# Optimization experiments

Hardware: AMD Instinct MI355X
Metric: run time of the kernel (lower is better)

The kernel has to match this reference:

```python
import jax, jax.numpy as jnp
import numpy as np

DIM = 1024
NUM_HEADS = 16
HEAD_DIM = DIM // NUM_HEADS
MLP_HIDDEN = 4 * DIM
TAU = 2.0
EPS = 1e-6
ALPHA_INIT = 0.01


def _xavier(key, out_f, in_f):
    limit = float(np.sqrt(6.0 / (in_f + out_f)))
    return jax.random.uniform(key, (out_f, in_f), jnp.float32, -limit, limit)


def setup_inputs() -> dict:
    key = jax.random.key(0)
    ks = jax.random.split(key, 10)
    B, Lq, Lkv = 4, 512, 2048
    return {
        "q_tokens": jax.random.normal(ks[0], (B, Lq, DIM), jnp.float32),
        "kv_tokens": jax.random.normal(ks[1], (B, Lkv, DIM), jnp.float32),
        "q_ln_w": jnp.ones((DIM,), jnp.float32),
        "q_ln_b": jnp.zeros((DIM,), jnp.float32),
        "kv_ln_w": jnp.ones((DIM,), jnp.float32),
        "kv_ln_b": jnp.zeros((DIM,), jnp.float32),
        "mlp_ln_w": jnp.ones((DIM,), jnp.float32),
        "mlp_ln_b": jnp.zeros((DIM,), jnp.float32),
        "Wq": _xavier(ks[2], DIM, DIM),
        "Wk": _xavier(ks[3], DIM, DIM),
        "Wv": _xavier(ks[4], DIM, DIM),
        "Wo": _xavier(ks[5], DIM, DIM),
        "bo": jnp.zeros((DIM,), jnp.float32),
        "fc1_w": _xavier(ks[6], MLP_HIDDEN, DIM),
        "fc1_b": jnp.zeros((MLP_HIDDEN,), jnp.float32),
        "fc2_w": _xavier(ks[7], DIM, MLP_HIDDEN),
        "fc2_b": jnp.zeros((DIM,), jnp.float32),
        "alpha_attn": jnp.full((1,), ALPHA_INIT, jnp.float32),
        "alpha_mlp": jnp.full((1,), ALPHA_INIT, jnp.float32),
    }


def _ln(x, w, b):
    mu = jnp.mean(x, axis=-1, keepdims=True)
    var = jnp.var(x, axis=-1, keepdims=True)
    return (x - mu) * jax.lax.rsqrt(var + EPS) * w + b


def _l2norm(x):
    # matches torch F.normalize: x / max(||x||, eps)
    n = jnp.sqrt(jnp.sum(x * x, axis=-1, keepdims=True))
    return x / jnp.maximum(n, EPS)


def reference(q_tokens, kv_tokens, q_ln_w, q_ln_b, kv_ln_w, kv_ln_b,
              mlp_ln_w, mlp_ln_b, Wq, Wk, Wv, Wo, bo,
              fc1_w, fc1_b, fc2_w, fc2_b, alpha_attn, alpha_mlp):
    B, Lq, D = q_tokens.shape
    q = _ln(q_tokens, q_ln_w, q_ln_b) @ Wq.T  # [B,Lq,D]
    kvn = _ln(kv_tokens, kv_ln_w, kv_ln_b)
    k = kvn @ Wk.T
    v = kvn @ Wv.T
    # split heads -> [B,H,L,hd]
    q = q.reshape(B, Lq, NUM_HEADS, HEAD_DIM)
    k = k.reshape(B, -1, NUM_HEADS, HEAD_DIM)
    v = v.reshape(B, -1, NUM_HEADS, HEAD_DIM)
    q = _l2norm(q)
    k = _l2norm(k)
    scores = jnp.einsum('bqhd,bkhd->bhqk', q, k) / TAU
    attn = jax.nn.softmax(scores, axis=-1)
    ctx = jnp.einsum('bhqk,bkhd->bqhd', attn, v).reshape(B, Lq, D)
    ctx = ctx @ Wo.T + bo
    out = q_tokens + alpha_attn * ctx
    h = _ln(out, mlp_ln_w, mlp_ln_b)
    h = jax.nn.gelu(h @ fc1_w.T + fc1_b, approximate=False)
    h = h @ fc2_w.T + fc2_b
    return out + alpha_mlp * h
```

## Files before the change

### kernel.cpp

```cpp
#include <hip/hip_runtime.h>


typedef __attribute__((ext_vector_type(8))) short short8_t;
typedef __attribute__((ext_vector_type(4))) float f32x4_t;

#define WSCALE 16.0f
#define OSC (1.0f / 16.0f)

__device__ __forceinline__ float b2f(short s) {
    union { float f; unsigned u; } c;
    c.u = ((unsigned)(unsigned short)s) << 16;
    return c.f;
}
__device__ __forceinline__ short f2b(float f) {
    union { float f; unsigned u; } c;
    c.f = f;
    unsigned u = c.u;
    unsigned r = (u + 0x7FFFu + ((u >> 16) & 1u)) >> 16;
    return (short)r;
}
__device__ __forceinline__ unsigned f2f8_pk4(float a, float b, float c, float d) {
    int lo = __builtin_amdgcn_cvt_pk_fp8_f32(a, b, 0, false);
    return (unsigned)__builtin_amdgcn_cvt_pk_fp8_f32(c, d, lo, true);
}
__device__ __forceinline__ unsigned char f2f8(float a) {
    return (unsigned char)(__builtin_amdgcn_cvt_pk_fp8_f32(a, a, 0, false) & 0xff);
}

__device__ __forceinline__ void gload16(const void* g, void* l) {
    __builtin_amdgcn_global_load_lds(
        (const __attribute__((address_space(1))) void*)g,
        (__attribute__((address_space(3))) void*)l, 16, 0, 0);
}

template <int OUT8>
__device__ __forceinline__ void ln_row(
    const float* __restrict__ x, const float* __restrict__ w,
    const float* __restrict__ bia, void* __restrict__ y,
    int row, int tid, float* red)
{
    const float4 t = *(const float4*)(x + (size_t)row * 1024 + tid * 4);
    float v[4] = {t.x, t.y, t.z, t.w};
    float s = v[0] + v[1] + v[2] + v[3];
    float s2 = v[0]*v[0] + v[1]*v[1] + v[2]*v[2] + v[3]*v[3];
    #pragma unroll
    for (int off = 1; off < 64; off <<= 1) {
        s  += __shfl_xor(s, off);
        s2 += __shfl_xor(s2, off);
    }
    const int wave = tid >> 6, lane = tid & 63;
    if (lane == 0) { red[wave] = s; red[4 + wave] = s2; }
    __syncthreads();
    s  = red[0] + red[1] + red[2] + red[3];
    s2 = red[4] + red[5] + red[6] + red[7];
    const float mu  = s * (1.0f / 1024.0f);
    const float var = s2 * (1.0f / 1024.0f) - mu * mu;
    const float rstd = rsqrtf(var + 1e-6f);
    const float4 wv = *(const float4*)(w + tid * 4);
    const float4 bv = *(const float4*)(bia + tid * 4);
    const float o0 = (v[0] - mu) * rstd * wv.x + bv.x;
    const float o1 = (v[1] - mu) * rstd * wv.y + bv.y;
    const float o2 = (v[2] - mu) * rstd * wv.z + bv.z;
    const float o3 = (v[3] - mu) * rstd * wv.w + bv.w;
    if (OUT8) {
        ((unsigned*)y)[(size_t)row * 256 + tid] = f2f8_pk4(o0, o1, o2, o3);
    } else {
        short4 o;
        o.x = f2b(o0); o.y = f2b(o1); o.z = f2b(o2); o.w = f2b(o3);
        *(short4*)((short*)y + (size_t)row * 1024 + tid * 4) = o;
    }
}

__global__ __launch_bounds__(256) void prep_kernel(
    const float* __restrict__ qt, const float* __restrict__ kvt,
    const float* __restrict__ qlw, const float* __restrict__ qlb,
    const float* __restrict__ klw, const float* __restrict__ klb,
    short* __restrict__ qn, unsigned char* __restrict__ kvn8,
    const float* __restrict__ Wq, const float* __restrict__ Wo,
    const float* __restrict__ Wk, const float* __restrict__ Wv,
    const float* __restrict__ fc1w, const float* __restrict__ fc2w,
    short* __restrict__ Wq_b, short* __restrict__ Wo_b,
    unsigned char* __restrict__ Wkv8,
    unsigned char* __restrict__ fc1_8, unsigned char* __restrict__ fc2_8)
{
    __shared__ float red[8];
    const int bid = blockIdx.x, tid = threadIdx.x;
    if (bid < 2048) {
        ln_row<0>(qt, qlw, qlb, qn, bid, tid, red);
    } else if (bid < 10240) {
        ln_row<1>(kvt, klw, klb, kvn8, bid - 2048, tid, red);
    } else {
        int f = (bid - 10240) * 256 + tid;
        if (f < 524288) {
            const float* src = (f < 262144) ? Wq : Wo;
            short* dst = (f < 262144) ? Wq_b : Wo_b;
            const int off = f & 262143;
            const float4 v = ((const float4*)src)[off];
            short4 o;
            o.x = f2b(v.x); o.y = f2b(v.y); o.z = f2b(v.z); o.w = f2b(v.w);
            ((short4*)dst)[off] = o;
        } else {
            const float* src; unsigned* dst; int off;
            if (f < 1048576) {
                off = f - 524288;
                src = (off < 262144) ? Wk : Wv;
                dst = (unsigned*)Wkv8;
                if (off >= 262144) { src = Wv; }
                const int so = (off < 262144) ? off : off - 262144;
                const float4 v = ((const float4*)src)[so];
                dst[off] = f2f8_pk4(v.x * WSCALE, v.y * WSCALE,
                                    v.z * WSCALE, v.w * WSCALE);
                return;
            } else if (f < 2097152) {
                off = f - 1048576; src = fc1w; dst = (unsigned*)fc1_8;
            } else {
                off = f - 2097152; src = fc2w; dst = (unsigned*)fc2_8;
            }
            const float4 v = ((const float4*)src)[off];
            dst[off] = f2f8_pk4(v.x * WSCALE, v.y * WSCALE,
                                v.z * WSCALE, v.w * WSCALE);
        }
    }
}

__global__ __launch_bounds__(256) void ln8_kernel(
    const float* __restrict__ x, const float* __restrict__ w,
    const float* __restrict__ bia, unsigned char* __restrict__ y)
{
    __shared__ float red[8];
    ln_row<1>(x, w, bia, y, blockIdx.x, threadIdx.x, red);
}

template <int EPI, int BM>
__global__ __launch_bounds__(256) void gemm_bt_kernel(
    const short* __restrict__ A, const short* __restrict__ W,
    int M, int N, int Ks, int Kst,
    const float* __restrict__ bias,
    const float* __restrict__ resF,
    const float* __restrict__ alpha,
    short* __restrict__ out16,
    float* __restrict__ outF)
{
    constexpr int MI = BM / 32;
    __shared__ __attribute__((aligned(16))) short As[2][BM * 64];
    __shared__ __attribute__((aligned(16))) short Bs[2][128 * 64];
    const int bm = blockIdx.y * BM, bn = blockIdx.x * 128;
    const int tid = threadIdx.x;
    const int wave = tid >> 6, lane = tid & 63;
    const int wm = (wave >> 1) * (BM / 2), wn = (wave & 1) * 64;
    const int l15 = lane & 15, quad = lane >> 4;
    const int l7 = l15 & 7;

    f32x4_t acc[MI][4];
    #pragma unroll
    for (int mi = 0; mi < MI; ++mi)
        #pragma unroll
        for (int ni = 0; ni < 4; ++ni)
            acc[mi][ni] = (f32x4_t){0.f, 0.f, 0.f, 0.f};

    auto stage = [&](int buf, int k0) {
        #pragma unroll
        for (int c = 0; c < BM / 32; ++c) {
            const int o = c * 4096 + tid * 16;
            const int row = o >> 7;
            const int g = ((o >> 4) & 7) ^ (row & 7);
            gload16(A + (size_t)(bm + row) * Kst + k0 + g * 8,
                    (char*)As[buf] + c * 4096 + wave * 1024);
        }
        #pragma unroll
        for (int c = 0; c < 4; ++c) {
            const int o = c * 4096 + tid * 16;
            const int row = o >> 7;
            const int g = ((o >> 4) & 7) ^ (row & 7);
            gload16(W + (size_t)(bn + row) * Kst + k0 + g * 8,
                    (char*)Bs[buf] + c * 4096 + wave * 1024);
        }
    };

    const int nIter = Ks >> 6;
    stage(0, 0);
    for (int it = 0; it < nIter; ++it) {
        const int buf = it & 1;
        __syncthreads();
        if (it + 1 < nIter) stage(buf ^ 1, (it + 1) * 64);
        #pragma unroll
        for (int h = 0; h < 2; ++h) {
            const int fg = (((h << 2) | quad) ^ l7) * 8;
            short8_t af[MI], bf[4];
            #pragma unroll
            for (int mi = 0; mi < MI; ++mi)
                af[mi] = *(const short8_t*)&As[buf][(wm + mi * 16 + l15) * 64 + fg];
            #pragma unroll
            for (int ni = 0; ni < 4; ++ni)
                bf[ni] = *(const short8_t*)&Bs[buf][(wn + ni * 16 + l15) * 64 + fg];
            #pragma unroll
            for (int mi = 0; mi < MI; ++mi)
                #pragma unroll
                for (int ni = 0; ni < 4; ++ni)
                    acc[mi][ni] = __builtin_amdgcn_mfma_f32_16x16x32_bf16(
                        af[mi], bf[ni], acc[mi][ni], 0, 0, 0);
        }
    }

    if (EPI == 4) {
        #pragma unroll
        for (int mi = 0; mi < MI; ++mi)
            #pragma unroll
            for (int r = 0; r < 4; ++r) {
                float s = 0.f;
                #pragma unroll
                for (int ni = 0; ni < 4; ++ni) {
                    const float x = acc[mi][ni][r];
                    s += x * x;
                }
                s += __shfl_xor(s, 1); s += __shfl_xor(s, 2);
                s += __shfl_xor(s, 4); s += __shfl_xor(s, 8);
                const float sc = 1.0f / fmaxf(sqrtf(s), 1e-6f);
                #pragma unroll
                for (int ni = 0; ni < 4; ++ni) acc[mi][ni][r] *= sc;
            }
    }

    const float a = (EPI == 1) ? alpha[0] : 0.f;
    #pragma unroll
    for (int mi = 0; mi < MI; ++mi) {
        #pragma unroll
        for (int ni = 0; ni < 4; ++ni) {
            const int n = bn + wn + ni * 16 + l15;
            const float bb = (EPI == 1) ? bias[n] : 0.f;
            #pragma unroll
            for (int r = 0; r < 4; ++r) {
                const int m = bm + wm + mi * 16 + (quad << 2) + r;
                const float x = acc[mi][ni][r];
                if (EPI == 4) {
                    out16[(size_t)m * N + n] = f2b(x);
                } else {
                    const size_t idx = (size_t)m * N + n;
                    outF[idx] = resF[idx] + a * (x + bb);
                }
            }
        }
    }
}

template <int EPI, int BM>
__global__ __launch_bounds__(256) void gemm_f8_kernel(
    const unsigned char* __restrict__ A, const unsigned char* __restrict__ W,
    int M, int N, int Ks, int Kst,
    const float* __restrict__ bias,
    unsigned char* __restrict__ out8,
    short* __restrict__ out16,
    float* __restrict__ outF)
{
    constexpr int MI = BM / 32;
    __shared__ __attribute__((aligned(16))) unsigned char pool[2 * BM * 128 + 2 * 128 * 128];
    auto AsBuf = [&](int b) { return pool + b * (BM * 128); };
    auto BsBuf = [&](int b) { return pool + 2 * BM * 128 + b * (128 * 128); };
    const int bm = blockIdx.y * BM, bn = blockIdx.x * 128;
    const size_t kbase = (size_t)blockIdx.z * Ks;
    const int tid = threadIdx.x;
    const int wave = tid >> 6, lane = tid & 63;
    const int wm = (wave >> 1) * (BM / 2), wn = (wave & 1) * 64;
    const int l15 = lane & 15, quad = lane >> 4;
    const int l7 = l15 & 7;

    f32x4_t acc[MI][4];
    #pragma unroll
    for (int mi = 0; mi < MI; ++mi)
        #pragma unroll
        for (int ni = 0; ni < 4; ++ni)
            acc[mi][ni] = (f32x4_t){0.f, 0.f, 0.f, 0.f};

    auto stage = [&](int buf, int k0) {
        #pragma unroll
        for (int c = 0; c < BM / 32; ++c) {
            const int o = c * 4096 + tid * 16;
            const int row = o >> 7;
            const int g = ((o >> 4) & 7) ^ (row & 7);
            gload16(A + (size_t)(bm + row) * Kst + kbase + k0 + g * 16,
                    (char*)AsBuf(buf) + c * 4096 + wave * 1024);
        }
        #pragma unroll
        for (int c = 0; c < 4; ++c) {
            const int o = c * 4096 + tid * 16;
            const int row = o >> 7;
            const int g = ((o >> 4) & 7) ^ (row & 7);
            gload16(W + (size_t)(bn + row) * Kst + kbase + k0 + g * 16,
                    (char*)BsBuf(buf) + c * 4096 + wave * 1024);
        }
    };

    const int nIter = Ks >> 7;
    stage(0, 0);
    for (int it = 0; it < nIter; ++it) {
        const int buf = it & 1;
        __syncthreads();
        if (it + 1 < nIter) stage(buf ^ 1, (it + 1) * 128);
        #pragma unroll
        for (int ks = 0; ks < 4; ++ks) {
            const int fo = ((((ks << 1) | (quad >> 1)) ^ l7) << 4) + (quad & 1) * 8;
            long af[MI], bf[4];
            #pragma unroll
            for (int mi = 0; mi < MI; ++mi)
                af[mi] = *(const long*)(AsBuf(buf) + (wm + mi * 16 + l15) * 128 + fo);
            #pragma unroll
            for (int ni = 0; ni < 4; ++ni)
                bf[ni] = *(const long*)(BsBuf(buf) + (wn + ni * 16 + l15) * 128 + fo);
            #pragma unroll
            for (int mi = 0; mi < MI; ++mi)
                #pragma unroll
                for (int ni = 0; ni < 4; ++ni)
                    acc[mi][ni] = __builtin_amdgcn_mfma_f32_16x16x32_fp8_fp8(
                        af[mi], bf[ni], acc[mi][ni], 0, 0, 0);
        }
    }

    if (EPI == 8) {
        const bool isK = (bn < 1024);
        if (isK) {
            #pragma unroll
            for (int mi = 0; mi < MI; ++mi)
                #pragma unroll
                for (int r = 0; r < 4; ++r) {
                    float s = 0.f;
                    #pragma unroll
                    for (int ni = 0; ni < 4; ++ni) {
                        const float x = acc[mi][ni][r];
                        s += x * x;
                    }
                    s += __shfl_xor(s, 1); s += __shfl_xor(s, 2);
                    s += __shfl_xor(s, 4); s += __shfl_xor(s, 8);
                    const float sc = 1.0f / fmaxf(sqrtf(s), 1e-6f);
                    #pragma unroll
                    for (int ni = 0; ni < 4; ++ni) acc[mi][ni][r] *= sc;
                }
        }
        __syncthreads();
        short* Ct = (short*)pool;
        constexpr int LDC = 136;
        if (isK) {
            #pragma unroll
            for (int mi = 0; mi < MI; ++mi)
                #pragma unroll
                for (int ni = 0; ni < 4; ++ni) {
                    const int n = wn + ni * 16 + l15;
                    #pragma unroll
                    for (int r = 0; r < 4; ++r)
                        Ct[(wm + mi * 16 + (quad << 2) + r) * LDC + n] =
                            f2b(acc[mi][ni][r]);
                }
        } else {
            #pragma unroll
            for (int mi = 0; mi < MI; ++mi)
                #pragma unroll
                for (int ni = 0; ni < 4; ++ni) {
                    short4 pk;
                    pk.x = f2b(acc[mi][ni][0] * OSC);
                    pk.y = f2b(acc[mi][ni][1] * OSC);
                    pk.z = f2b(acc[mi][ni][2] * OSC);
                    pk.w = f2b(acc[mi][ni][3] * OSC);
                    *(short4*)&Ct[(wn + ni * 16 + l15) * LDC +
                                  wm + mi * 16 + (quad << 2)] = pk;
                }
        }
        __syncthreads();
        const int b_ = bm >> 11;
        const int kv0 = bm & 2047;
        #pragma unroll
        for (int p = 0; p < 8; ++p) {
            const int idx = p * 256 + tid;
            const int row = idx >> 4, ch = idx & 15;
            const short8_t v = *(const short8_t*)&Ct[row * LDC + ch * 8];
            if (isK) {
                const int hh = (bn >> 6) + (ch >> 3);
                *(short8_t*)&out16[(size_t)((b_ * 16 + hh) * 2048 + kv0 + row) * 64 +
                                   (ch & 7) * 8] = v;
            } else {
                const int nn = bn - 1024 + row;
                *(short8_t*)&((short*)outF)[(size_t)((b_ * 16 + (nn >> 6)) * 64 +
                                            (nn & 63)) * 2048 + kv0 + ch * 8] = v;
            }
        }
        return;
    }

    if (EPI == 2) {
        __syncthreads();
        unsigned char* C8 = (unsigned char*)pool;
        constexpr int LDC8 = 144;
        #pragma unroll
        for (int mi = 0; mi < MI; ++mi)
            #pragma unroll
            for (int ni = 0; ni < 4; ++ni) {
                const int n = wn + ni * 16 + l15;
                const float bb = bias[bn + n];
                #pragma unroll
                for (int r = 0; r < 4; ++r) {
                    const float t = acc[mi][ni][r] * OSC + bb;
                    C8[(wm + mi * 16 + (quad << 2) + r) * LDC8 + n] =
                        f2f8(0.5f * t * (1.0f + erff(t * 0.70710678118f)));
                }
            }
        __syncthreads();
        #pragma unroll
        for (int p = 0; p < 4; ++p) {
            const int idx = p * 256 + tid;
            const int row = idx >> 3, ch = idx & 7;
            const f32x4_t v = *(const f32x4_t*)&C8[row * LDC8 + ch * 16];
            *(f32x4_t*)&out8[(size_t)(bm + row) * N + bn + ch * 16] = v;
        }
        return;
    }

    #pragma unroll
    for (int mi = 0; mi < MI; ++mi) {
        #pragma unroll
        for (int ni = 0; ni < 4; ++ni) {
            const int n = bn + wn + ni * 16 + l15;
            #pragma unroll
            for (int r = 0; r < 4; ++r) {
                const int m = bm + wm + mi * 16 + (quad << 2) + r;
                outF[(size_t)blockIdx.z * M * N + (size_t)m * N + n] =
                    acc[mi][ni][r];
            }
        }
    }
}

__global__ __launch_bounds__(256) void reduce4_kernel(
    const float* __restrict__ parts, const float* __restrict__ resF,
    const float* __restrict__ bias, const float* __restrict__ alpha,
    float* __restrict__ out)
{
    const int i = blockIdx.x * 256 + threadIdx.x;
    const size_t MN4 = (size_t)2048 * 1024 / 4;
    const float a = alpha[0];
    const float4 b4 = ((const float4*)bias)[i & 255];
    float4 s = ((const float4*)parts)[i];
    const float4 p1 = ((const float4*)parts)[MN4 + i];
    const float4 p2 = ((const float4*)parts)[2 * MN4 + i];
    const float4 p3 = ((const float4*)parts)[3 * MN4 + i];
    const float4 rv = ((const float4*)resF)[i];
    float4 o;
    o.x = rv.x + a * ((s.x + p1.x + p2.x + p3.x) * OSC + b4.x);
    o.y = rv.y + a * ((s.y + p1.y + p2.y + p3.y) * OSC + b4.y);
    o.z = rv.z + a * ((s.z + p1.z + p2.z + p3.z) * OSC + b4.z);
    o.w = rv.w + a * ((s.w + p1.w + p2.w + p3.w) * OSC + b4.w);
    ((float4*)out)[i] = o;
}

__global__ __launch_bounds__(256) void attn_kernel(
    const short* __restrict__ q, const short* __restrict__ khd,
    const short* __restrict__ vhd, float* __restrict__ o0,
    float* __restrict__ o1, float* __restrict__ lpart)
{
    const int h  = blockIdx.x;
    const int b  = blockIdx.y;
    const int qt = blockIdx.z >> 1;
    const int sp = blockIdx.z & 1;
    const int tid = threadIdx.x;
    const int wave = tid >> 6, lane = tid & 63;
    const int l15 = lane & 15, quad = lane >> 4;
    const int q0 = qt * 64 + wave * 16;
    const int t0 = sp * 16;

    __shared__ __attribute__((aligned(16))) short Ks[2][4096];
    __shared__ __attribute__((aligned(16))) short Vs[2][4096];
    __shared__ __attribute__((aligned(16))) short P[4][1152];

    const short* qbase = q + (size_t)(b * 512 + q0 + l15) * 1024 + h * 64 + quad * 8;
    const short8_t aq0 = *(const short8_t*)(qbase);
    const short8_t aq1 = *(const short8_t*)(qbase + 32);

    const short* kbase = khd + (size_t)(b * 16 + h) * 2048 * 64;
    const short* vbase = vhd + (size_t)(b * 16 + h) * 64 * 2048;

    const int swz = l15 & 7;
    const int g0 = (quad ^ swz) * 8;
    const int g1 = ((quad ^ swz) ^ 4) * 8;

    auto stage = [&](int buf, int t) {
        #pragma unroll
        for (int c = 0; c < 2; ++c) {
            const int o = c * 4096 + tid * 16;
            const int row = o >> 7;
            const int g = ((o >> 4) & 7) ^ (row & 7);
            gload16(kbase + (size_t)(t * 64 + row) * 64 + g * 8,
                    (char*)Ks[buf] + c * 4096 + wave * 1024);
            gload16(vbase + (size_t)row * 2048 + t * 64 + g * 8,
                    (char*)Vs[buf] + c * 4096 + wave * 1024);
        }
    };

    const short8_t ones = {(short)0x3F80, (short)0x3F80, (short)0x3F80,
                           (short)0x3F80, (short)0x3F80, (short)0x3F80,
                           (short)0x3F80, (short)0x3F80};

    f32x4_t oacc[4];
    #pragma unroll
    for (int u = 0; u < 4; ++u) oacc[u] = (f32x4_t){0.f, 0.f, 0.f, 0.f};
    f32x4_t lacc = (f32x4_t){0.f, 0.f, 0.f, 0.f};

    stage(0, t0);
    for (int tt = 0; tt < 16; ++tt) {
        const int buf = tt & 1;
        __syncthreads();
        if (tt + 1 < 16) stage(buf ^ 1, t0 + tt + 1);

        f32x4_t s[4];
        #pragma unroll
        for (int ss = 0; ss < 4; ++ss) {
            const int R = ss * 16 + l15;
            const short8_t bk0 = *(const short8_t*)&Ks[buf][R * 64 + g0];
            const short8_t bk1 = *(const short8_t*)&Ks[buf][R * 64 + g1];
            f32x4_t a = (f32x4_t){0.f, 0.f, 0.f, 0.f};
            a = __builtin_amdgcn_mfma_f32_16x16x32_bf16(aq0, bk0, a, 0, 0, 0);
            a = __builtin_amdgcn_mfma_f32_16x16x32_bf16(aq1, bk1, a, 0, 0, 0);
            s[ss] = a;
        }
        #pragma unroll
        for (int ss = 0; ss < 4; ++ss)
            #pragma unroll
            for (int r = 0; r < 4; ++r) {
                const float p = __expf(s[ss][r] * 0.5f);
                P[wave][(quad * 4 + r) * 72 + ss * 16 + l15] = f2b(p);
            }
        const short8_t ap0 = *(const short8_t*)&P[wave][l15 * 72 + quad * 8];
        const short8_t ap1 = *(const short8_t*)&P[wave][l15 * 72 + 32 + quad * 8];
        lacc = __builtin_amdgcn_mfma_f32_16x16x32_bf16(ap0, ones, lacc, 0, 0, 0);
        lacc = __builtin_amdgcn_mfma_f32_16x16x32_bf16(ap1, ones, lacc, 0, 0, 0);
        #pragma unroll
        for (int u = 0; u < 4; ++u) {
            const int R = u * 16 + l15;
            const short8_t bv0 = *(const short8_t*)&Vs[buf][R * 64 + g0];
            const short8_t bv1 = *(const short8_t*)&Vs[buf][R * 64 + g1];
            oacc[u] = __builtin_amdgcn_mfma_f32_16x16x32_bf16(ap0, bv0, oacc[u], 0, 0, 0);
            oacc[u] = __builtin_amdgcn_mfma_f32_16x16x32_bf16(ap1, bv1, oacc[u], 0, 0, 0);
        }
    }

    float* ob = sp ? o1 : o0;
    float* lb = lpart + (size_t)sp * 2048 * 16;
    #pragma unroll
    for (int u = 0; u < 4; ++u)
        #pragma unroll
        for (int r = 0; r < 4; ++r)
            ob[(size_t)(b * 512 + q0 + quad * 4 + r) * 1024 + h * 64 + u * 16 + l15] =
                oacc[u][r];
    if (l15 == 0) {
        #pragma unroll
        for (int r = 0; r < 4; ++r)
            lb[(size_t)(b * 512 + q0 + quad * 4 + r) * 16 + h] = lacc[r];
    }
}

__global__ __launch_bounds__(256) void attn_combine_kernel(
    const float* __restrict__ o0, const float* __restrict__ o1,
    const float* __restrict__ lpart, short* __restrict__ ctx)
{
    const int i = blockIdx.x * 256 + threadIdx.x;
    const int row = i >> 8;
    const int h = (i & 255) >> 4;
    const float l = lpart[row * 16 + h] + lpart[2048 * 16 + row * 16 + h];
    const float inv = 1.0f / l;
    const float4 a = ((const float4*)o0)[i];
    const float4 c = ((const float4*)o1)[i];
    short4 o;
    o.x = f2b((a.x + c.x) * inv);
    o.y = f2b((a.y + c.y) * inv);
    o.z = f2b((a.z + c.z) * inv);
    o.w = f2b((a.w + c.w) * inv);
    ((short4*)ctx)[i] = o;
}

extern "C" void kernel_launch(void* const* d_in, const int* in_sizes, int n_in,
                              void* d_out, int out_size, void* d_ws, size_t ws_size,
                              hipStream_t stream)
{
    const float* q_tokens  = (const float*)d_in[0];
    const float* kv_tokens = (const float*)d_in[1];
    const float* q_ln_w    = (const float*)d_in[2];
    const float* q_ln_b    = (const float*)d_in[3];
    const float* kv_ln_w   = (const float*)d_in[4];
    const float* kv_ln_b   = (const float*)d_in[5];
    const float* mlp_ln_w  = (const float*)d_in[6];
    const float* mlp_ln_b  = (const float*)d_in[7];
    const float* Wq        = (const float*)d_in[8];
    const float* Wk        = (const float*)d_in[9];
    const float* Wv        = (const float*)d_in[10];
    const float* Wo        = (const float*)d_in[11];
    const float* bo        = (const float*)d_in[12];
    const float* fc1_w     = (const float*)d_in[13];
    const float* fc1_b     = (const float*)d_in[14];
    const float* fc2_w     = (const float*)d_in[15];
    const float* fc2_b     = (const float*)d_in[16];
    const float* alpha_attn = (const float*)d_in[17];
    const float* alpha_mlp  = (const float*)d_in[18];

    char* ws = (char*)d_ws;
    const size_t MB = (size_t)1 << 20;
    short* khd    = (short*)(ws);
    short* vhd    = (short*)(ws + 16 * MB);
    float* parts  = (float*)(ws);
    unsigned char* kvn8 = (unsigned char*)(ws + 32 * MB);
    float* attn_o0 = (float*)(ws + 32 * MB);
    unsigned char* h1   = (unsigned char*)(ws + 32 * MB);
    short* qn     = (short*)(ws + 40 * MB);
    short* qbuf   = (short*)(ws + 44 * MB);
    short* ctx    = (short*)(ws + 48 * MB);
    float* aout   = (float*)(ws + 52 * MB);
    float* attn_o1 = (float*)(ws + 52 * MB);
    unsigned char* hn8 = (unsigned char*)(ws + 60 * MB);
    float* attn_l  = (float*)(ws + 60 * MB);
    short* Wq_b   = (short*)(ws + 62 * MB);
    short* Wo_b   = (short*)(ws + 64 * MB);
    unsigned char* Wkv8  = (unsigned char*)(ws + 66 * MB);
    unsigned char* fc1_8 = (unsigned char*)(ws + 68 * MB);
    unsigned char* fc2_8 = (unsigned char*)(ws + 72 * MB);

    prep_kernel<<<22528, 256, 0, stream>>>(
        q_tokens, kv_tokens, q_ln_w, q_ln_b, kv_ln_w, kv_ln_b, qn, kvn8,
        Wq, Wo, Wk, Wv, fc1_w, fc2_w,
        Wq_b, Wo_b, Wkv8, fc1_8, fc2_8);

    gemm_bt_kernel<4, 64><<<dim3(8, 32), 256, 0, stream>>>(
        qn, Wq_b, 2048, 1024, 1024, 1024, nullptr, nullptr, nullptr, qbuf, nullptr);
    gemm_f8_kernel<8, 128><<<dim3(16, 64), 256, 0, stream>>>(
        kvn8, Wkv8, 8192, 2048, 1024, 1024, nullptr, nullptr, khd, (float*)vhd);

    attn_kernel<<<dim3(16, 4, 16), 256, 0, stream>>>(
        qbuf, khd, vhd, attn_o0, attn_o1, attn_l);
    attn_combine_kernel<<<2048, 256, 0, stream>>>(attn_o0, attn_o1, attn_l, ctx);

    gemm_bt_kernel<1, 64><<<dim3(8, 32), 256, 0, stream>>>(
        ctx, Wo_b, 2048, 1024, 1024, 1024, bo, q_tokens, alpha_attn, nullptr, aout);

    ln8_kernel<<<2048, 256, 0, stream>>>(aout, mlp_ln_w, mlp_ln_b, hn8);

    gemm_f8_kernel<2, 128><<<dim3(32, 16), 256, 0, stream>>>(
        hn8, fc1_8, 2048, 4096, 1024, 1024, fc1_b, h1, nullptr, nullptr);

    gemm_f8_kernel<7, 64><<<dim3(8, 32, 4), 256, 0, stream>>>(
        h1, fc2_8, 2048, 1024, 1024, 4096, nullptr, nullptr, nullptr, parts);
    reduce4_kernel<<<2048, 256, 0, stream>>>(parts, aout, fc2_b, alpha_mlp,
                                             (float*)d_out);
}
```

Before: 326.0 us.

## Keep attention probabilities in registers via transposed QK MFMA and 16x16x16 PV

The QK^T MFMA operands are swapped so each lane's score accumulator already matches the A-operand layout of a 16x16x16 bf16 MFMA. The probabilities are packed to bf16 in registers with v_cvt_pk_bf16_f32 and fed straight into the row-sum and PV MFMAs. This removes the per-wave LDS scratch for P and its write/read round trip. The trade is twice as many smaller MFMA instructions, narrower V reads from LDS, and a launch-bounds hint of 4 blocks per SM that may constrain registers.

New measurement: 312.3 us. 1.04x faster.

```diff
diff --git a/kernel.cpp b/kernel.cpp
--- a/kernel.cpp
+++ b/kernel.cpp
@@ -2,6 +2,7 @@
 
 
 typedef __attribute__((ext_vector_type(8))) short short8_t;
+typedef __attribute__((ext_vector_type(4))) short short4_t;
 typedef __attribute__((ext_vector_type(4))) float f32x4_t;
 
 #define WSCALE 16.0f
@@ -18,6 +19,11 @@
     unsigned u = c.u;
     unsigned r = (u + 0x7FFFu + ((u >> 16) & 1u)) >> 16;
     return (short)r;
+}
+__device__ __forceinline__ unsigned cvt_pk_bf16(float lo, float hi) {
+    unsigned r;
+    asm("v_cvt_pk_bf16_f32 %0, %1, %2" : "=v"(r) : "v"(lo), "v"(hi));
+    return r;
 }
 __device__ __forceinline__ unsigned f2f8_pk4(float a, float b, float c, float d) {
     int lo = __builtin_amdgcn_cvt_pk_fp8_f32(a, b, 0, false);
@@ -449,7 +455,7 @@
     ((float4*)out)[i] = o;
 }
 
-__global__ __launch_bounds__(256) void attn_kernel(
+__global__ __launch_bounds__(256, 4) void attn_kernel(
     const short* __restrict__ q, const short* __restrict__ khd,
     const short* __restrict__ vhd, float* __restrict__ o0,
     float* __restrict__ o1, float* __restrict__ lpart)
@@ -466,7 +472,6 @@
 
     __shared__ __attribute__((aligned(16))) short Ks[2][4096];
     __shared__ __attribute__((aligned(16))) short Vs[2][4096];
-    __shared__ __attribute__((aligned(16))) short P[4][1152];
 
     const short* qbase = q + (size_t)(b * 512 + q0 + l15) * 1024 + h * 64 + quad * 8;
     const short8_t aq0 = *(const short8_t*)(qbase);
@@ -492,9 +497,8 @@
         }
     };
 
-    const short8_t ones = {(short)0x3F80, (short)0x3F80, (short)0x3F80,
-                           (short)0x3F80, (short)0x3F80, (short)0x3F80,
-                           (short)0x3F80, (short)0x3F80};
+    const short4_t ones4 = {(short)0x3F80, (short)0x3F80,
+                            (short)0x3F80, (short)0x3F80};
 
     f32x4_t oacc[4];
     #pragma unroll
@@ -514,28 +518,36 @@
             const short8_t bk0 = *(const short8_t*)&Ks[buf][R * 64 + g0];
             const short8_t bk1 = *(const short8_t*)&Ks[buf][R * 64 + g1];
             f32x4_t a = (f32x4_t){0.f, 0.f, 0.f, 0.f};
-            a = __builtin_amdgcn_mfma_f32_16x16x32_bf16(aq0, bk0, a, 0, 0, 0);
-            a = __builtin_amdgcn_mfma_f32_16x16x32_bf16(aq1, bk1, a, 0, 0, 0);
+            a = __builtin_amdgcn_mfma_f32_16x16x32_bf16(bk0, aq0, a, 0, 0, 0);
+            a = __builtin_amdgcn_mfma_f32_16x16x32_bf16(bk1, aq1, a, 0, 0, 0);
             s[ss] = a;
         }
+        short4_t pa[4];
+        #pragma unroll
+        for (int ss = 0; ss < 4; ++ss) {
+            const float p0 = __expf(s[ss][0] * 0.5f);
+            const float p1 = __expf(s[ss][1] * 0.5f);
+            const float p2 = __expf(s[ss][2] * 0.5f);
+            const float p3 = __expf(s[ss][3] * 0.5f);
+            union { unsigned w[2]; short4_t v; } u_;
+            u_.w[0] = cvt_pk_bf16(p0, p1);
+            u_.w[1] = cvt_pk_bf16(p2, p3);
+            pa[ss] = u_.v;
+        }
         #pragma unroll
         for (int ss = 0; ss < 4; ++ss)
-            #pragma unroll
-            for (int r = 0; r < 4; ++r) {
-                const float p = __expf(s[ss][r] * 0.5f);
-                P[wave][(quad * 4 + r) * 72 + ss * 16 + l15] = f2b(p);
+            lacc = __builtin_amdgcn_mfma_f32_16x16x16bf16_1k(
+                pa[ss], ones4, lacc, 0, 0, 0);
+        #pragma unroll
+        for (int ss = 0; ss < 4; ++ss) {
+            const int ch = (((ss * 2 + (quad >> 1)) ^ swz) << 3) + ((quad & 1) << 2);
+            #pragma unroll
+            for (int u = 0; u < 4; ++u) {
+                const short4_t bv =
+                    *(const short4_t*)&Vs[buf][(u * 16 + l15) * 64 + ch];
+                oacc[u] = __builtin_amdgcn_mfma_f32_16x16x16bf16_1k(
+                    pa[ss], bv, oacc[u], 0, 0, 0);
             }
-        const short8_t ap0 = *(const short8_t*)&P[wave][l15 * 72 + quad * 8];
-        const short8_t ap1 = *(const short8_t*)&P[wave][l15 * 72 + 32 + quad * 8];
-        lacc = __builtin_amdgcn_mfma_f32_16x16x32_bf16(ap0, ones, lacc, 0, 0, 0);
-        lacc = __builtin_amdgcn_mfma_f32_16x16x32_bf16(ap1, ones, lacc, 0, 0, 0);
-        #pragma unroll
-        for (int u = 0; u < 4; ++u) {
-            const int R = u * 16 + l15;
-            const short8_t bv0 = *(const short8_t*)&Vs[buf][R * 64 + g0];
-            const short8_t bv1 = *(const short8_t*)&Vs[buf][R * 64 + g1];
-            oacc[u] = __builtin_amdgcn_mfma_f32_16x16x32_bf16(ap0, bv0, oacc[u], 0, 0, 0);
-            oacc[u] = __builtin_amdgcn_mfma_f32_16x16x32_bf16(ap1, bv1, oacc[u], 0, 0, 0);
         }
     }
 
```
